# Optimization experiments

Measured on AMD Instinct MI355X. Metric: run time of the kernel, lower is better.

The kernel has to match this reference:

```python
import jax, jax.numpy as jnp
import numpy as np

N = 50000   # num_nodes
E = 400000  # random edges (avg degree 8)


def setup_inputs() -> dict:
    key = jax.random.key(0)
    ks = jax.random.split(key, 12)

    def w(k, shape):
        # xavier-ish scaling
        return (jax.random.normal(k, shape, jnp.float32)
                / jnp.sqrt(jnp.float32(shape[0])))

    return {
        "node_emb": jax.random.normal(ks[0], (N, 128), jnp.float32) * 0.05,
        "edge_index": jax.random.randint(ks[1], (2, E), 0, N, dtype=jnp.int32),
        "W1": w(ks[2], (128, 512)), "b1": jnp.zeros((512,), jnp.float32),
        "W2": w(ks[3], (512, 128)), "b2": jnp.zeros((128,), jnp.float32),
        "Wres": w(ks[4], (512, 128)), "bres": jnp.zeros((128,), jnp.float32),
        "Wfc1": w(ks[5], (128, 256)), "bfc1": jnp.zeros((256,), jnp.float32),
        "Wfc2": w(ks[6], (256, 1)), "bfc2": jnp.zeros((1,), jnp.float32),
    }


def reference(node_emb, edge_index, W1, b1, W2, b2, Wres, bres,
              Wfc1, bfc1, Wfc2, bfc2):
    n = node_emb.shape[0]
    loops = jnp.arange(n, dtype=edge_index.dtype)
    # explicit add_self_loops in forward + GCNConv's internal gcn_norm self
    # loops => each node gets TWO self loops (faithful to the torch code).
    src = jnp.concatenate([edge_index[0], loops, loops])
    dst = jnp.concatenate([edge_index[1], loops, loops])

    deg = jax.ops.segment_sum(jnp.ones(src.shape, node_emb.dtype), dst,
                              num_segments=n)
    dinv = jnp.where(deg > 0, jax.lax.rsqrt(deg), 0.0)
    norm = dinv[src] * dinv[dst]  # [Etot]

    def gcn(x, W, b):
        h = x @ W                                    # [N, out]
        msg = h[src] * norm[:, None]                 # gather + scale
        agg = jax.ops.segment_sum(msg, dst, num_segments=n)  # scatter-add
        return agg + b

    x1 = jax.nn.relu(gcn(node_emb, W1, b1))   # [N, 512] (dropout = eval/id)
    x2 = jax.nn.relu(gcn(x1, W2, b2))          # [N, 128]
    x = x2 + x1 @ Wres + bres                  # residual projection
    A = jax.nn.relu(x @ Wfc1 + bfc1) @ Wfc2 + bfc2  # [N, 1]
    return (x, A)
```

## Files before the change

kernel.cpp:

```cpp
#include <hip/hip_runtime.h>


typedef unsigned short u16;
typedef short bf16x8 __attribute__((ext_vector_type(8)));
typedef unsigned short us8 __attribute__((ext_vector_type(8)));
typedef float f32x4 __attribute__((ext_vector_type(4)));

static inline int cdiv_ll(long long a, long long b) { return (int)((a + b - 1) / b); }

__device__ inline float bf2f(u16 u) {
    union { unsigned int i; float f; } v; v.i = ((unsigned int)u) << 16; return v.f;
}
__device__ inline u16 f2bf(float x) {
    union { float f; unsigned int i; } v; v.f = x;
    unsigned int r = v.i + 0x7fffu + ((v.i >> 16) & 1u);
    return (u16)(r >> 16);
}


__global__ __launch_bounds__(256) void setup_kernel(const float* __restrict__ emb,
                                                    const float* __restrict__ W1,
                                                    const float* __restrict__ W2,
                                                    const float* __restrict__ Wres,
                                                    const float* __restrict__ Wfc1,
                                                    const float* __restrict__ bfc2,
                                                    u16* __restrict__ embb,
                                                    u16* __restrict__ W1t,
                                                    u16* __restrict__ Wct,
                                                    u16* __restrict__ Wfc1t,
                                                    int* __restrict__ cnt,
                                                    float* __restrict__ Aout,
                                                    int N) {
    long long r = (long long)blockIdx.x * 256 + threadIdx.x;
    const long long nf2b = (long long)N * 32;
    if (r < nf2b) {
        float4 v = ((const float4*)emb)[r];
        uint2 o;
        o.x = (unsigned)f2bf(v.x) | ((unsigned)f2bf(v.y) << 16);
        o.y = (unsigned)f2bf(v.z) | ((unsigned)f2bf(v.w) << 16);
        ((uint2*)embb)[r] = o;
        return;
    }
    r -= nf2b;
    if (r < 512 * 128) {
        int n = (int)(r / 128), k = (int)(r % 128);
        W1t[r] = f2bf(W1[(size_t)k * 512 + n]);
        return;
    }
    r -= 512 * 128;
    if (r < 256 * 512) {
        int n = (int)(r / 512), k = (int)(r % 512);
        float v = (n < 128) ? W2[(size_t)k * 128 + n] : Wres[(size_t)k * 128 + (n - 128)];
        Wct[r] = f2bf(v);
        return;
    }
    r -= 256 * 512;
    if (r < 256 * 128) {
        int n = (int)(r / 128), k = (int)(r % 128);
        Wfc1t[r] = f2bf(Wfc1[(size_t)k * 256 + n]);
        return;
    }
    r -= 256 * 128;
    if (r < N) { cnt[(int)r] = 0; return; }
    r -= N;
    if (r < N) Aout[(int)r] = bfc2[0];
}


__global__ __launch_bounds__(256) void hist_kernel(const int* __restrict__ dst,
                                                   int* __restrict__ cnt, int E) {
    int e = blockIdx.x * 256 + threadIdx.x;
    if (e < E) atomicAdd(&cnt[dst[e]], 1);
}

__global__ __launch_bounds__(256) void scanA_kernel(const int* __restrict__ cnt,
                                                    int* __restrict__ excl,
                                                    int* __restrict__ bsum, int N) {
    __shared__ int tmp[256];
    int i = blockIdx.x * 256 + threadIdx.x;
    int v = (i < N) ? cnt[i] : 0;
    tmp[threadIdx.x] = v;
    __syncthreads();
    for (int o = 1; o < 256; o <<= 1) {
        int t = (threadIdx.x >= (unsigned)o) ? tmp[threadIdx.x - o] : 0;
        __syncthreads();
        tmp[threadIdx.x] += t;
        __syncthreads();
    }
    if (i < N) excl[i] = tmp[threadIdx.x] - v;
    if (threadIdx.x == 255) bsum[blockIdx.x] = tmp[255];
}

__global__ __launch_bounds__(256) void scanC2_kernel(const int* __restrict__ excl,
                                                     const int* __restrict__ bsum,
                                                     const int* __restrict__ cnt,
                                                     int* __restrict__ rowptr,
                                                     int* __restrict__ cursor,
                                                     float* __restrict__ dinv,
                                                     int N, int E) {
    __shared__ int tmp[256];
    int t = threadIdx.x;
    tmp[t] = (t < (int)blockIdx.x) ? bsum[t] : 0;
    __syncthreads();
    for (int o = 128; o; o >>= 1) {
        if (t < o) tmp[t] += tmp[t + o];
        __syncthreads();
    }
    int pre = tmp[0];
    int i = blockIdx.x * 256 + t;
    if (i < N) {
        int r = excl[i] + pre;
        rowptr[i] = r;
        cursor[i] = r;
        dinv[i] = rsqrtf((float)cnt[i] + 2.0f);
    }
    if (i == 0) rowptr[N] = E;
}

__global__ __launch_bounds__(256) void fill_kernel(const int* __restrict__ src,
                                                   const int* __restrict__ dst,
                                                   const float* __restrict__ dinv,
                                                   int* __restrict__ cursor,
                                                   int* __restrict__ csr_src,
                                                   float* __restrict__ csr_w, int E) {
    int e = blockIdx.x * 256 + threadIdx.x;
    if (e >= E) return;
    int s = src[e], d = dst[e];
    int idx = atomicAdd(&cursor[d], 1);
    csr_src[idx] = s;
    csr_w[idx] = dinv[s] * dinv[d];
}


#define AGG_EDGE(SR, WR)                                                       \
    {                                                                          \
        unsigned int vv = hp[(size_t)(SR) * 64 + lane];                        \
        ax = fmaf(bf2f((u16)vv), (WR), ax);                                    \
        ay = fmaf(bf2f((u16)(vv >> 16)), (WR), ay);                            \
    }

__device__ inline void agg_row(const unsigned int* __restrict__ hp,
                               const int* __restrict__ rowptr,
                               const int* __restrict__ csr_src,
                               const float* __restrict__ csr_w,
                               const float* __restrict__ dinv,
                               int wid, int lane, float& ax, float& ay) {
    float dv = dinv[wid];
    unsigned int hv = hp[(size_t)wid * 64 + lane];
    float c0 = 2.0f * dv * dv;
    ax = bf2f((u16)hv) * c0;
    ay = bf2f((u16)(hv >> 16)) * c0;
    int e = rowptr[wid], e1 = rowptr[wid + 1];
    for (; e + 7 < e1; e += 8) {
        int s0 = csr_src[e + 0], s1 = csr_src[e + 1], s2 = csr_src[e + 2], s3 = csr_src[e + 3];
        int s4 = csr_src[e + 4], s5 = csr_src[e + 5], s6 = csr_src[e + 6], s7 = csr_src[e + 7];
        float w0 = csr_w[e + 0], w1 = csr_w[e + 1], w2 = csr_w[e + 2], w3 = csr_w[e + 3];
        float w4 = csr_w[e + 4], w5 = csr_w[e + 5], w6 = csr_w[e + 6], w7 = csr_w[e + 7];
        AGG_EDGE(s0, w0); AGG_EDGE(s1, w1); AGG_EDGE(s2, w2); AGG_EDGE(s3, w3);
        AGG_EDGE(s4, w4); AGG_EDGE(s5, w5); AGG_EDGE(s6, w6); AGG_EDGE(s7, w7);
    }
    if (e + 3 < e1) {
        int s0 = csr_src[e + 0], s1 = csr_src[e + 1], s2 = csr_src[e + 2], s3 = csr_src[e + 3];
        float w0 = csr_w[e + 0], w1 = csr_w[e + 1], w2 = csr_w[e + 2], w3 = csr_w[e + 3];
        AGG_EDGE(s0, w0); AGG_EDGE(s1, w1); AGG_EDGE(s2, w2); AGG_EDGE(s3, w3);
        e += 4;
    }
    for (; e < e1; ++e) {
        int s0 = csr_src[e]; float w0 = csr_w[e];
        AGG_EDGE(s0, w0);
    }
}

__global__ __launch_bounds__(256) void aggb_kernel(const u16* __restrict__ hb,
                                                   const int* __restrict__ rowptr,
                                                   const int* __restrict__ csr_src,
                                                   const float* __restrict__ csr_w,
                                                   const float* __restrict__ dinv,
                                                   u16* __restrict__ out, int N) {
    int wid  = (blockIdx.x * blockDim.x + threadIdx.x) >> 6;
    int lane = threadIdx.x & 63;
    if (wid >= N) return;
    float ax, ay;
    agg_row((const unsigned int*)hb, rowptr, csr_src, csr_w, dinv, wid, lane, ax, ay);
    ((unsigned int*)out)[(size_t)wid * 64 + lane] =
        (unsigned)f2bf(ax) | ((unsigned)f2bf(ay) << 16);
}

__global__ __launch_bounds__(256) void aggfin_kernel(const u16* __restrict__ hb,
                                                     const int* __restrict__ rowptr,
                                                     const int* __restrict__ csr_src,
                                                     const float* __restrict__ csr_w,
                                                     const float* __restrict__ dinv,
                                                     const float* __restrict__ b2,
                                                     const float* __restrict__ bres,
                                                     float* __restrict__ xout, int N) {
    int wid  = (blockIdx.x * blockDim.x + threadIdx.x) >> 6;
    int lane = threadIdx.x & 63;
    if (wid >= N) return;
    float ax, ay;
    agg_row((const unsigned int*)hb, rowptr, csr_src, csr_w, dinv, wid, lane, ax, ay);
    float2 bb = ((const float2*)b2)[lane];
    float2 rr = ((const float2*)bres)[lane];
    float2 hres = ((float2*)xout)[(size_t)wid * 64 + lane];
    float ox = fmaxf(ax + bb.x, 0.f) + hres.x + rr.x;
    float oy = fmaxf(ay + bb.y, 0.f) + hres.y + rr.y;
    ((float2*)xout)[(size_t)wid * 64 + lane] = make_float2(ox, oy);
}


__global__ __launch_bounds__(256) void mgemm12(const u16* __restrict__ aggE,
                                               const u16* __restrict__ W1t,
                                               const u16* __restrict__ Wct,
                                               const float* __restrict__ b1,
                                               int M,
                                               u16* __restrict__ h2b,
                                               float* __restrict__ xout) {
    extern __shared__ u16 X1s[];
    const int LD = 136;
    const int t = threadIdx.x;
    const int bm = blockIdx.x * 64;
    const int wn = t >> 6;
    const int lane = t & 63;
    const int l15 = lane & 15, lg = lane >> 4;

    bf16x8 afr[4][4];
#pragma unroll
    for (int ks = 0; ks < 4; ++ks)
#pragma unroll
        for (int fm = 0; fm < 4; ++fm) {
            int row = bm + 16 * fm + l15;
            bf16x8 v = (bf16x8)(short)0;
            if (row < M)
                v = *(const bf16x8*)(aggE + (size_t)row * 128 + 32 * ks + 8 * lg);
            afr[ks][fm] = v;
        }

    f32x4 acc2[4][4];
#pragma unroll
    for (int i = 0; i < 4; ++i)
#pragma unroll
        for (int j = 0; j < 4; ++j) acc2[i][j] = (f32x4)(0.0f);

    for (int p = 0; p < 4; ++p) {
        __syncthreads();

        f32x4 acc1[4][2];
#pragma unroll
        for (int i = 0; i < 4; ++i)
#pragma unroll
            for (int j = 0; j < 2; ++j) acc1[i][j] = (f32x4)(0.0f);
#pragma unroll
        for (int ks = 0; ks < 4; ++ks) {
            bf16x8 wfr[2];
#pragma unroll
            for (int fn = 0; fn < 2; ++fn)
                wfr[fn] = *(const bf16x8*)(W1t +
                    (size_t)(128 * p + 32 * wn + 16 * fn + l15) * 128 + 32 * ks + 8 * lg);
#pragma unroll
            for (int fm = 0; fm < 4; ++fm)
#pragma unroll
                for (int fn = 0; fn < 2; ++fn)
                    acc1[fm][fn] = __builtin_amdgcn_mfma_f32_16x16x32_bf16(
                        wfr[fn], afr[ks][fm], acc1[fm][fn], 0, 0, 0);
        }

#pragma unroll
        for (int fm = 0; fm < 4; ++fm) {
#pragma unroll
            for (int fn = 0; fn < 2; ++fn) {
                int col1 = 32 * wn + 16 * fn + 4 * lg;
                float4 b4 = *(const float4*)&b1[128 * p + col1];
                f32x4 v = acc1[fm][fn];
                float v0 = fmaxf(v[0] + b4.x, 0.f), v1 = fmaxf(v[1] + b4.y, 0.f);
                float v2 = fmaxf(v[2] + b4.z, 0.f), v3 = fmaxf(v[3] + b4.w, 0.f);
                uint2 o;
                o.x = (unsigned)f2bf(v0) | ((unsigned)f2bf(v1) << 16);
                o.y = (unsigned)f2bf(v2) | ((unsigned)f2bf(v3) << 16);
                *(uint2*)&X1s[(16 * fm + l15) * LD + col1] = o;
            }
        }

        bf16x8 wfr2[4][4];
#pragma unroll
        for (int ks = 0; ks < 4; ++ks)
#pragma unroll
            for (int fn = 0; fn < 4; ++fn)
                wfr2[ks][fn] = *(const bf16x8*)(Wct +
                    (size_t)(64 * wn + 16 * fn + l15) * 512 + 128 * p + 32 * ks + 8 * lg);

        __syncthreads();

#pragma unroll
        for (int ks = 0; ks < 4; ++ks) {
            bf16x8 xfr[4];
#pragma unroll
            for (int fm = 0; fm < 4; ++fm)
                xfr[fm] = *(const bf16x8*)&X1s[(16 * fm + l15) * LD + 32 * ks + 8 * lg];
#pragma unroll
            for (int fm = 0; fm < 4; ++fm)
#pragma unroll
                for (int fn = 0; fn < 4; ++fn)
                    acc2[fm][fn] = __builtin_amdgcn_mfma_f32_16x16x32_bf16(
                        wfr2[ks][fn], xfr[fm], acc2[fm][fn], 0, 0, 0);
        }
    }

#pragma unroll
    for (int fm = 0; fm < 4; ++fm) {
        const int row = bm + 16 * fm + l15;
        if (row >= M) continue;
#pragma unroll
        for (int fn = 0; fn < 4; ++fn) {
            const int col = 64 * wn + 16 * fn + 4 * lg;
            f32x4 v = acc2[fm][fn];
            if (col < 128) {
                uint2 o;
                o.x = (unsigned)f2bf(v[0]) | ((unsigned)f2bf(v[1]) << 16);
                o.y = (unsigned)f2bf(v[2]) | ((unsigned)f2bf(v[3]) << 16);
                *(uint2*)(h2b + (size_t)row * 128 + col) = o;
            } else {
                *(float4*)(xout + (size_t)row * 128 + (col - 128)) =
                    make_float4(v[0], v[1], v[2], v[3]);
            }
        }
    }
}


__global__ __launch_bounds__(512) void head_gemm(const float* __restrict__ X,
                                                 const u16* __restrict__ Bt,
                                                 int M,
                                                 const float* __restrict__ bias,
                                                 const float* __restrict__ w2,
                                                 float* __restrict__ Cf) {
    __shared__ u16 As[128][72];
    __shared__ u16 Bs[256][72];
    const int t = threadIdx.x;
    const int bm = blockIdx.x * 128;
    const int w = t >> 6, lane = t & 63;
    const int wm = w >> 2, wn = w & 3;
    const int l15 = lane & 15, lg = lane >> 4;
    const int srow = t >> 3, scol = (t & 7) * 8;
    const int K = 128;

    f32x4 acc[4][4];
#pragma unroll
    for (int i = 0; i < 4; ++i)
#pragma unroll
        for (int j = 0; j < 4; ++j) acc[i][j] = (f32x4)(0.0f);

    for (int kk = 0; kk < K; kk += 64) {
#pragma unroll
        for (int i = 0; i < 2; ++i) {
            int row = srow + 64 * i;
            uint4 o = make_uint4(0u, 0u, 0u, 0u);
            if (bm + row < M) {
                const float* src = X + (size_t)(bm + row) * K + kk + scol;
                float4 a = *(const float4*)src;
                float4 b = *(const float4*)(src + 4);
                o.x = (unsigned)f2bf(a.x) | ((unsigned)f2bf(a.y) << 16);
                o.y = (unsigned)f2bf(a.z) | ((unsigned)f2bf(a.w) << 16);
                o.z = (unsigned)f2bf(b.x) | ((unsigned)f2bf(b.y) << 16);
                o.w = (unsigned)f2bf(b.z) | ((unsigned)f2bf(b.w) << 16);
            }
            *(uint4*)&As[row][scol] = o;
        }
#pragma unroll
        for (int i = 0; i < 4; ++i) {
            int row = srow + 64 * i;
            *(us8*)&Bs[row][scol] =
                *(const us8*)(Bt + (size_t)row * K + kk + scol);
        }
        __syncthreads();
#pragma unroll
        for (int ks = 0; ks < 2; ++ks) {
            const int ko = 32 * ks + lg * 8;
            bf16x8 bfr[4], afr[4];
#pragma unroll
            for (int fn = 0; fn < 4; ++fn)
                bfr[fn] = *(const bf16x8*)&Bs[64 * wn + 16 * fn + l15][ko];
#pragma unroll
            for (int fm = 0; fm < 4; ++fm)
                afr[fm] = *(const bf16x8*)&As[64 * wm + 16 * fm + l15][ko];
#pragma unroll
            for (int fm = 0; fm < 4; ++fm)
#pragma unroll
                for (int fn = 0; fn < 4; ++fn)
                    acc[fm][fn] = __builtin_amdgcn_mfma_f32_16x16x32_bf16(
                        bfr[fn], afr[fm], acc[fm][fn], 0, 0, 0);
        }
        __syncthreads();
    }

    float4 bl4[4], wl4[4];
#pragma unroll
    for (int fn = 0; fn < 4; ++fn) {
        int c = 64 * wn + 16 * fn + 4 * lg;
        bl4[fn] = *(const float4*)&bias[c];
        wl4[fn] = *(const float4*)&w2[c];
    }
#pragma unroll
    for (int fm = 0; fm < 4; ++fm) {
        float p = 0.f;
#pragma unroll
        for (int fn = 0; fn < 4; ++fn) {
            p += fmaxf(acc[fm][fn][0] + bl4[fn].x, 0.f) * wl4[fn].x;
            p += fmaxf(acc[fm][fn][1] + bl4[fn].y, 0.f) * wl4[fn].y;
            p += fmaxf(acc[fm][fn][2] + bl4[fn].z, 0.f) * wl4[fn].z;
            p += fmaxf(acc[fm][fn][3] + bl4[fn].w, 0.f) * wl4[fn].w;
        }
        p += __shfl_xor(p, 16);
        p += __shfl_xor(p, 32);
        int row = bm + 64 * wm + 16 * fm + l15;
        if (lane < 16 && row < M) atomicAdd(&Cf[row], p);
    }
}


extern "C" void kernel_launch(void* const* d_in, const int* in_sizes, int n_in,
                              void* d_out, int out_size, void* d_ws, size_t ws_size,
                              hipStream_t stream) {
    const float* emb  = (const float*)d_in[0];
    const int*   eidx = (const int*)d_in[1];
    const float* W1   = (const float*)d_in[2];
    const float* b1   = (const float*)d_in[3];
    const float* W2   = (const float*)d_in[4];
    const float* b2   = (const float*)d_in[5];
    const float* Wres = (const float*)d_in[6];
    const float* bres = (const float*)d_in[7];
    const float* Wfc1 = (const float*)d_in[8];
    const float* bfc1 = (const float*)d_in[9];
    const float* Wfc2 = (const float*)d_in[10];
    const float* bfc2 = (const float*)d_in[11];

    const int N = in_sizes[0] / 128;
    const int E = in_sizes[1] / 2;
    const int* srcv = eidx;
    const int* dstv = eidx + E;

    float* out  = (float*)d_out;
    float* xout = out;
    float* Aout = out + (size_t)N * 128;

    char* p = (char*)d_ws;
    float* dinv  = (float*)p;            p += (size_t)N * 4;
    float* csr_w = (float*)p;            p += (size_t)E * 4;
    u16*  embb   = (u16*)p;              p += (size_t)N * 128 * 2;
    u16*  aggEb  = (u16*)p;              p += (size_t)N * 128 * 2;
    u16*  h2b    = (u16*)p;              p += (size_t)N * 128 * 2;
    u16*  W1t    = (u16*)p;              p += (size_t)512 * 128 * 2;
    u16*  Wct    = (u16*)p;              p += (size_t)256 * 512 * 2;
    u16*  Wfc1t  = (u16*)p;              p += (size_t)256 * 128 * 2;
    int*  cnt     = (int*)p;             p += (size_t)N * 4;
    int*  excl    = (int*)p;             p += (size_t)N * 4;
    int*  rowptr  = (int*)p;             p += (size_t)(N + 1) * 4;
    int*  cursor  = (int*)p;             p += (size_t)N * 4;
    int*  bsum    = (int*)p;             p += 256 * 4;
    int*  csr_src = (int*)p;             p += (size_t)E * 4;

    const int T  = 256;
    const int nb = cdiv_ll(N, 256);

    const long long setup_work = (long long)N * 32 + 512 * 128 + 256 * 512
                               + 256 * 128 + (long long)N + (long long)N;
    setup_kernel<<<cdiv_ll(setup_work, T), T, 0, stream>>>(
        emb, W1, W2, Wres, Wfc1, bfc2, embb, W1t, Wct, Wfc1t, cnt, Aout, N);

    hist_kernel<<<cdiv_ll(E, T), T, 0, stream>>>(dstv, cnt, E);
    scanA_kernel<<<nb, T, 0, stream>>>(cnt, excl, bsum, N);
    scanC2_kernel<<<nb, T, 0, stream>>>(excl, bsum, cnt, rowptr, cursor, dinv, N, E);
    fill_kernel<<<cdiv_ll(E, T), T, 0, stream>>>(srcv, dstv, dinv, cursor, csr_src, csr_w, E);

    aggb_kernel<<<cdiv_ll((long long)N * 64, T), T, 0, stream>>>(
        embb, rowptr, csr_src, csr_w, dinv, aggEb, N);

    const size_t lds12 = (size_t)(64 * 136) * sizeof(u16);
    mgemm12<<<cdiv_ll(N, 64), 256, lds12, stream>>>(
        aggEb, W1t, Wct, b1, N, h2b, xout);

    aggfin_kernel<<<cdiv_ll((long long)N * 64, T), T, 0, stream>>>(
        h2b, rowptr, csr_src, csr_w, dinv, b2, bres, xout, N);

    head_gemm<<<cdiv_ll(N, 128), 512, 0, stream>>>(
        xout, Wfc1t, N, bfc1, Wfc2, Aout);
}
```

Baseline: 205.6 us.

## Chain the fused two-GEMM kernel in registers per wave, removing the LDS staging

The fused GEMM1→GEMM2 kernel now gives each wave 16 nodes and keeps the whole 512-wide hidden row in registers. The GEMM1 output layout is fed directly as the B operand of a 16x16x16 MFMA for GEMM2, so the LDS buffer and both barriers go away. In exchange, each wave reloads the full W1 and Wct weights from global/L2 instead of splitting the columns across four waves. It also uses half-K MFMAs with narrow 8-byte weight loads, which raises weight traffic and instruction count per node.

```diff
diff --git a/kernel.cpp b/kernel.cpp
--- a/kernel.cpp
+++ b/kernel.cpp
@@ -3,6 +3,7 @@
 
 typedef unsigned short u16;
 typedef short bf16x8 __attribute__((ext_vector_type(8)));
+typedef short bf16x4 __attribute__((ext_vector_type(4)));
 typedef unsigned short us8 __attribute__((ext_vector_type(8)));
 typedef float f32x4 __attribute__((ext_vector_type(4)));
 
@@ -215,111 +216,71 @@
                                                int M,
                                                u16* __restrict__ h2b,
                                                float* __restrict__ xout) {
-    extern __shared__ u16 X1s[];
-    const int LD = 136;
     const int t = threadIdx.x;
-    const int bm = blockIdx.x * 64;
-    const int wn = t >> 6;
+    const int wv = t >> 6;
     const int lane = t & 63;
     const int l15 = lane & 15, lg = lane >> 4;
-
-    bf16x8 afr[4][4];
-#pragma unroll
-    for (int ks = 0; ks < 4; ++ks)
-#pragma unroll
-        for (int fm = 0; fm < 4; ++fm) {
-            int row = bm + 16 * fm + l15;
-            bf16x8 v = (bf16x8)(short)0;
-            if (row < M)
-                v = *(const bf16x8*)(aggE + (size_t)row * 128 + 32 * ks + 8 * lg);
-            afr[ks][fm] = v;
-        }
-
-    f32x4 acc2[4][4];
-#pragma unroll
-    for (int i = 0; i < 4; ++i)
-#pragma unroll
-        for (int j = 0; j < 4; ++j) acc2[i][j] = (f32x4)(0.0f);
+    const int node = blockIdx.x * 64 + wv * 16 + l15;
+
+    bf16x8 afr[4];
+#pragma unroll
+    for (int ks = 0; ks < 4; ++ks) {
+        bf16x8 v = (bf16x8)(short)0;
+        if (node < M)
+            v = *(const bf16x8*)(aggE + (size_t)node * 128 + 32 * ks + 8 * lg);
+        afr[ks] = v;
+    }
+
+    f32x4 acc2[16];
+#pragma unroll
+    for (int i = 0; i < 16; ++i) acc2[i] = (f32x4)(0.0f);
 
     for (int p = 0; p < 4; ++p) {
-        __syncthreads();
-
-        f32x4 acc1[4][2];
-#pragma unroll
-        for (int i = 0; i < 4; ++i)
-#pragma unroll
-            for (int j = 0; j < 2; ++j) acc1[i][j] = (f32x4)(0.0f);
+        f32x4 acc1[8];
+#pragma unroll
+        for (int i = 0; i < 8; ++i) acc1[i] = (f32x4)(0.0f);
 #pragma unroll
         for (int ks = 0; ks < 4; ++ks) {
-            bf16x8 wfr[2];
-#pragma unroll
-            for (int fn = 0; fn < 2; ++fn)
-                wfr[fn] = *(const bf16x8*)(W1t +
-                    (size_t)(128 * p + 32 * wn + 16 * fn + l15) * 128 + 32 * ks + 8 * lg);
-#pragma unroll
-            for (int fm = 0; fm < 4; ++fm)
-#pragma unroll
-                for (int fn = 0; fn < 2; ++fn)
-                    acc1[fm][fn] = __builtin_amdgcn_mfma_f32_16x16x32_bf16(
-                        wfr[fn], afr[ks][fm], acc1[fm][fn], 0, 0, 0);
-        }
-
-#pragma unroll
-        for (int fm = 0; fm < 4; ++fm) {
-#pragma unroll
-            for (int fn = 0; fn < 2; ++fn) {
-                int col1 = 32 * wn + 16 * fn + 4 * lg;
-                float4 b4 = *(const float4*)&b1[128 * p + col1];
-                f32x4 v = acc1[fm][fn];
-                float v0 = fmaxf(v[0] + b4.x, 0.f), v1 = fmaxf(v[1] + b4.y, 0.f);
-                float v2 = fmaxf(v[2] + b4.z, 0.f), v3 = fmaxf(v[3] + b4.w, 0.f);
-                uint2 o;
-                o.x = (unsigned)f2bf(v0) | ((unsigned)f2bf(v1) << 16);
-                o.y = (unsigned)f2bf(v2) | ((unsigned)f2bf(v3) << 16);
-                *(uint2*)&X1s[(16 * fm + l15) * LD + col1] = o;
+#pragma unroll
+            for (int q = 0; q < 8; ++q) {
+                bf16x8 w1f = *(const bf16x8*)(W1t +
+                    (size_t)(128 * p + 16 * q + l15) * 128 + 32 * ks + 8 * lg);
+                acc1[q] = __builtin_amdgcn_mfma_f32_16x16x32_bf16(
+                    w1f, afr[ks], acc1[q], 0, 0, 0);
             }
         }
 
-        bf16x8 wfr2[4][4];
-#pragma unroll
-        for (int ks = 0; ks < 4; ++ks)
-#pragma unroll
-            for (int fn = 0; fn < 4; ++fn)
-                wfr2[ks][fn] = *(const bf16x8*)(Wct +
-                    (size_t)(64 * wn + 16 * fn + l15) * 512 + 128 * p + 32 * ks + 8 * lg);
-
-        __syncthreads();
-
-#pragma unroll
-        for (int ks = 0; ks < 4; ++ks) {
-            bf16x8 xfr[4];
-#pragma unroll
-            for (int fm = 0; fm < 4; ++fm)
-                xfr[fm] = *(const bf16x8*)&X1s[(16 * fm + l15) * LD + 32 * ks + 8 * lg];
-#pragma unroll
-            for (int fm = 0; fm < 4; ++fm)
-#pragma unroll
-                for (int fn = 0; fn < 4; ++fn)
-                    acc2[fm][fn] = __builtin_amdgcn_mfma_f32_16x16x32_bf16(
-                        wfr2[ks][fn], xfr[fm], acc2[fm][fn], 0, 0, 0);
-        }
-    }
-
-#pragma unroll
-    for (int fm = 0; fm < 4; ++fm) {
-        const int row = bm + 16 * fm + l15;
-        if (row >= M) continue;
-#pragma unroll
-        for (int fn = 0; fn < 4; ++fn) {
-            const int col = 64 * wn + 16 * fn + 4 * lg;
-            f32x4 v = acc2[fm][fn];
+#pragma unroll
+        for (int q = 0; q < 8; ++q) {
+            const int c1 = 128 * p + 16 * q + 4 * lg;
+            float4 b4 = *(const float4*)&b1[c1];
+            bf16x4 xf;
+            xf[0] = (short)f2bf(fmaxf(acc1[q][0] + b4.x, 0.f));
+            xf[1] = (short)f2bf(fmaxf(acc1[q][1] + b4.y, 0.f));
+            xf[2] = (short)f2bf(fmaxf(acc1[q][2] + b4.z, 0.f));
+            xf[3] = (short)f2bf(fmaxf(acc1[q][3] + b4.w, 0.f));
+#pragma unroll
+            for (int fn2 = 0; fn2 < 16; ++fn2) {
+                bf16x4 w2f = *(const bf16x4*)(Wct +
+                    (size_t)(16 * fn2 + l15) * 512 + c1);
+                acc2[fn2] = __builtin_amdgcn_mfma_f32_16x16x16bf16_1k(
+                    w2f, xf, acc2[fn2], 0, 0, 0);
+            }
+        }
+    }
+
+    if (node < M) {
+#pragma unroll
+        for (int fn2 = 0; fn2 < 16; ++fn2) {
+            const int col = 16 * fn2 + 4 * lg;
+            f32x4 v = acc2[fn2];
             if (col < 128) {
                 uint2 o;
                 o.x = (unsigned)f2bf(v[0]) | ((unsigned)f2bf(v[1]) << 16);
                 o.y = (unsigned)f2bf(v[2]) | ((unsigned)f2bf(v[3]) << 16);
-                *(uint2*)(h2b + (size_t)row * 128 + col) = o;
+                *(uint2*)(h2b + (size_t)node * 128 + col) = o;
             } else {
-                *(float4*)(xout + (size_t)row * 128 + (col - 128)) =
+                *(float4*)(xout + (size_t)node * 128 + (col - 128)) =
                     make_float4(v[0], v[1], v[2], v[3]);
             }
         }
@@ -474,8 +435,7 @@
     aggb_kernel<<<cdiv_ll((long long)N * 64, T), T, 0, stream>>>(
         embb, rowptr, csr_src, csr_w, dinv, aggEb, N);
 
-    const size_t lds12 = (size_t)(64 * 136) * sizeof(u16);
-    mgemm12<<<cdiv_ll(N, 64), 256, lds12, stream>>>(
+    mgemm12<<<cdiv_ll(N, 64), 256, 0, stream>>>(
         aggEb, W1t, Wct, b1, N, h2b, xout);
 
     aggfin_kernel<<<cdiv_ll((long long)N * 64, T), T, 0, stream>>>(
```

Result: slower. 437.7 us (+112.9%).
